# Kernel tuning notes

Hardware: AMD Instinct MI355X
Metric: run time of the kernel (lower is better)

The kernel has to match this reference:

```python
import jax, jax.numpy as jnp
import numpy as np
import math

EMBED_DIM = 1024
NUM_HEADS = 16
QK_DIM = 64
SCALE = 1.0 / math.sqrt(QK_DIM)  # beta=None -> 1/sqrt(qk_dim)


def setup_inputs() -> dict:
    key = jax.random.key(0)
    k1, k2, k3 = jax.random.split(key, 3)
    hidden_states = jax.random.normal(k1, (2, 2048, EMBED_DIM), dtype=jnp.float32)
    # nn.init.normal_(std=0.002)
    query_proj = 0.002 * jax.random.normal(k2, (NUM_HEADS, QK_DIM, EMBED_DIM), dtype=jnp.float32)
    key_proj = 0.002 * jax.random.normal(k3, (NUM_HEADS, QK_DIM, EMBED_DIM), dtype=jnp.float32)
    query_bias = jnp.zeros((QK_DIM,), dtype=jnp.float32)
    key_bias = jnp.zeros((QK_DIM,), dtype=jnp.float32)
    return {
        "hidden_states": hidden_states,
        "query_proj": query_proj,
        "key_proj": key_proj,
        "query_bias": query_bias,
        "key_bias": key_bias,
    }


def reference(hidden_states, query_proj, key_proj, query_bias, key_bias):
    # queries/keys: [b, n, h, q]
    queries = jnp.einsum("bnd,hqd->bnhq", hidden_states, query_proj) + query_bias
    keys = jnp.einsum("bnd,hqd->bnhq", hidden_states, key_proj) + key_bias
    # scores: [b, h, n, m]
    scores = jnp.einsum("bnhq,bmhq->bhnm", queries, keys)
    # energy: -sum logsumexp over last dim, divided by scale
    lse = jax.scipy.special.logsumexp(SCALE * scores, axis=-1)
    return -jnp.sum(lse) / SCALE
```

## Files before the change

kernel.cpp:

```cpp
#include <hip/hip_runtime.h>
#include <hip/hip_bf16.h>
#include <stdint.h>


typedef __bf16 bf16_t;
typedef bf16_t bf16x8 __attribute__((ext_vector_type(8)));
typedef float f32x4 __attribute__((ext_vector_type(4)));
typedef float f32x16 __attribute__((ext_vector_type(16)));

#define MFMA16(a,b,c) __builtin_amdgcn_mfma_f32_16x16x32_bf16(a,b,c,0,0,0)
#define MFMA32(a,b,c) __builtin_amdgcn_mfma_f32_32x32x16_bf16(a,b,c,0,0,0)
#define GLL16(g, l) __builtin_amdgcn_global_load_lds(                       \
    (const __attribute__((address_space(1))) void*)(g),                     \
    (__attribute__((address_space(3))) void*)(l), 16, 0, 0)

static constexpr int SEQ = 2048, BATCH = 2, EMBED = 1024, NH = 16, QKD = 64;
static constexpr int M_TOT = BATCH * SEQ;
static constexpr int N_TOT = 2 * NH * QKD;
static constexpr float C1 = 0.125f * 1.44269504088896340736f;

__global__ __launch_bounds__(256) void cvt_kernel(
    const float* __restrict__ hs, const float* __restrict__ qp,
    const float* __restrict__ kp, bf16_t* __restrict__ hsb,
    bf16_t* __restrict__ projb)
{
    int i = blockIdx.x * 256 + threadIdx.x;
    const float* src; bf16_t* dst;
    if (i < 524288) { src = hs + (size_t)i * 8; dst = hsb + (size_t)i * 8; }
    else {
        int j = i - 524288;
        dst = projb + (size_t)j * 8;
        src = (j < 131072) ? qp + (size_t)j * 8 : kp + (size_t)(j - 131072) * 8;
    }
    f32x4 a = ((const f32x4*)src)[0], b = ((const f32x4*)src)[1];
    bf16x8 r;
    r[0]=(bf16_t)a[0]; r[1]=(bf16_t)a[1]; r[2]=(bf16_t)a[2]; r[3]=(bf16_t)a[3];
    r[4]=(bf16_t)b[0]; r[5]=(bf16_t)b[1]; r[6]=(bf16_t)b[2]; r[7]=(bf16_t)b[3];
    *(bf16x8*)dst = r;
}

__global__ __launch_bounds__(256) void proj_kernel(
    const bf16_t* __restrict__ A, const bf16_t* __restrict__ B,
    const float* __restrict__ qb, const float* __restrict__ kb,
    bf16_t* __restrict__ C)
{
    __shared__ __align__(16) char sA[2][16384];
    __shared__ __align__(16) char sB[2][16384];
    const int t = threadIdx.x, lane = t & 63, wv = t >> 6;
    const int bid = blockIdx.x;
    const int xcd = bid & 7, idx = bid >> 3;
    const int am0 = (xcd * 4 + (idx >> 4)) * 128;
    const int bn0 = (idx & 15) * 128;
    const int wr = wv >> 1, wc = wv & 1;
    const int l15 = lane & 15, g = lane >> 4;

    const int srow = wv * 8 + (lane >> 3);
    const int sgr  = (lane & 7) ^ ((lane >> 3) & 7);
    const bf16_t* ga = A + (size_t)(am0 + srow) * EMBED + sgr * 8;
    const bf16_t* gb = B + (size_t)(bn0 + srow) * EMBED + sgr * 8;
    const int lbase = wv * 1024;

    f32x4 acc[4][4] = {};

#pragma unroll
    for (int is = 0; is < 4; ++is) {
        GLL16(ga + (size_t)is * 32 * EMBED, &sA[0][lbase + is * 4096]);
        GLL16(gb + (size_t)is * 32 * EMBED, &sB[0][lbase + is * 4096]);
    }
    __syncthreads();

    int cur = 0;
    for (int kk = 0; kk < EMBED; kk += 64) {
        if (kk + 64 < EMBED) {
#pragma unroll
            for (int is = 0; is < 4; ++is) {
                GLL16(ga + kk + 64 + (size_t)is * 32 * EMBED, &sA[cur ^ 1][lbase + is * 4096]);
                GLL16(gb + kk + 64 + (size_t)is * 32 * EMBED, &sB[cur ^ 1][lbase + is * 4096]);
            }
        }
#pragma unroll
        for (int s = 0; s < 2; ++s) {
            bf16x8 af[4], bfv[4];
#pragma unroll
            for (int mt = 0; mt < 4; ++mt) {
                int row = wr * 64 + mt * 16 + l15;
                af[mt] = *(const bf16x8*)&sA[cur][row * 128 + 16 * (((s << 2) | g) ^ (row & 7))];
            }
#pragma unroll
            for (int nt = 0; nt < 4; ++nt) {
                int row = wc * 64 + nt * 16 + l15;
                bfv[nt] = *(const bf16x8*)&sB[cur][row * 128 + 16 * (((s << 2) | g) ^ (row & 7))];
            }
#pragma unroll
            for (int mt = 0; mt < 4; ++mt)
#pragma unroll
                for (int nt = 0; nt < 4; ++nt)
                    acc[mt][nt] = MFMA16(af[mt], bfv[nt], acc[mt][nt]);
        }
        __syncthreads();
        cur ^= 1;
    }

#pragma unroll
    for (int nt = 0; nt < 4; ++nt) {
        int col = bn0 + wc * 64 + nt * 16 + l15;
        float bias, scale;
        if (col < NH * QKD) { bias = qb[col & 63]; scale = C1; }
        else                { bias = kb[col & 63]; scale = 1.0f; }
#pragma unroll
        for (int mt = 0; mt < 4; ++mt)
#pragma unroll
            for (int j = 0; j < 4; ++j) {
                int row = am0 + wr * 64 + mt * 16 + g * 4 + j;
                C[(size_t)row * N_TOT + col] = (bf16_t)((acc[mt][nt][j] + bias) * scale);
            }
    }
}

__global__ __launch_bounds__(256) void lse_kernel(
    const bf16_t* __restrict__ qk, float* __restrict__ partials)
{
    __shared__ float rows_s[4][128];
    __shared__ float ws[4];
    const int t = threadIdx.x, lane = t & 63, wv = t >> 6;
    const int bid = blockIdx.x;
    const int xcd = bid & 7, idx = bid >> 3;
    const int pair = xcd * 4 + (idx >> 4);
    const int tile = idx & 15;
    const int b = pair >> 4, h = pair & 15;
    const int qr0 = tile * 128;
    const int l31 = lane & 31, g5 = lane >> 5;
    const size_t base = (size_t)b * SEQ;

    bf16x8 qf[4][4];
#pragma unroll
    for (int mt = 0; mt < 4; ++mt) {
        const bf16_t* qp_ = qk + (base + qr0 + mt * 32 + l31) * N_TOT + h * QKD + g5 * 8;
#pragma unroll
        for (int kf = 0; kf < 4; ++kf)
            qf[mt][kf] = *(const bf16x8*)(qp_ + kf * 16);
    }

    const bf16_t* kb_ = qk + (base + wv * 512 + l31) * N_TOT + NH * QKD + h * QKD + g5 * 8;

    float sume[4] = {0.f, 0.f, 0.f, 0.f};

    bf16x8 kv[4];
#pragma unroll
    for (int kf = 0; kf < 4; ++kf) kv[kf] = *(const bf16x8*)(kb_ + kf * 16);

    for (int ct = 0; ct < 16; ++ct) {
        bf16x8 kn[4];
        const bf16_t* kn_p = kb_ + (size_t)((ct < 15 ? ct + 1 : 15) * 32) * N_TOT;
#pragma unroll
        for (int kf = 0; kf < 4; ++kf) kn[kf] = *(const bf16x8*)(kn_p + kf * 16);

        f32x16 sacc[4];
#pragma unroll
        for (int mt = 0; mt < 4; ++mt) {
            f32x16 z = {};
            sacc[mt] = z;
#pragma unroll
            for (int kf = 0; kf < 4; ++kf)
                sacc[mt] = MFMA32(kv[kf], qf[mt][kf], sacc[mt]);
        }
#pragma unroll
        for (int mt = 0; mt < 4; ++mt) {
            float e = 0.f;
#pragma unroll
            for (int j = 0; j < 16; ++j)
                e += __builtin_amdgcn_exp2f(sacc[mt][j]);
            sume[mt] += e;
        }
#pragma unroll
        for (int kf = 0; kf < 4; ++kf) kv[kf] = kn[kf];
    }

#pragma unroll
    for (int mt = 0; mt < 4; ++mt) {
        float v = sume[mt] + __shfl_xor(sume[mt], 32);
        if (g5 == 0) rows_s[wv][mt * 32 + l31] = v;
    }
    __syncthreads();

    float lg = 0.f;
    if (t < 128) {
        float tot = rows_s[0][t] + rows_s[1][t] + rows_s[2][t] + rows_s[3][t];
        lg = __builtin_amdgcn_logf(tot);
    }
#pragma unroll
    for (int m = 1; m < 64; m <<= 1) lg += __shfl_xor(lg, m);
    if (lane == 0) ws[wv] = lg;
    __syncthreads();
    if (t == 0)
        partials[bid] = ws[0] + ws[1] + ws[2] + ws[3];
}

__global__ __launch_bounds__(256) void final_kernel(
    const float* __restrict__ partials, int n, float* __restrict__ out)
{
    float s = 0.f;
    for (int i = threadIdx.x; i < n; i += 256) s += partials[i];
#pragma unroll
    for (int m = 1; m < 64; m <<= 1) s += __shfl_xor(s, m);
    __shared__ float wsf[4];
    const int wave = threadIdx.x >> 6, lane = threadIdx.x & 63;
    if (lane == 0) wsf[wave] = s;
    __syncthreads();
    if (threadIdx.x == 0)
        out[0] = -8.0f * 0.69314718055994530942f * (wsf[0] + wsf[1] + wsf[2] + wsf[3]);
}

extern "C" void kernel_launch(void* const* d_in, const int* in_sizes, int n_in,
                              void* d_out, int out_size, void* d_ws, size_t ws_size,
                              hipStream_t stream)
{
    const float* hs = (const float*)d_in[0];
    const float* qp = (const float*)d_in[1];
    const float* kp = (const float*)d_in[2];
    const float* qb = (const float*)d_in[3];
    const float* kb = (const float*)d_in[4];

    bf16_t* hsb   = (bf16_t*)d_ws;
    bf16_t* projb = hsb + (size_t)M_TOT * EMBED;
    bf16_t* qkb   = projb + (size_t)N_TOT * EMBED;
    float*  partials = (float*)(qkb + (size_t)M_TOT * N_TOT);
    float*  out = (float*)d_out;

    cvt_kernel<<<3072, 256, 0, stream>>>(hs, qp, kp, hsb, projb);
    proj_kernel<<<512, 256, 0, stream>>>(hsb, projb, qb, kb, qkb);
    lse_kernel<<<512, 256, 0, stream>>>(qkb, partials);
    final_kernel<<<1, 256, 0, stream>>>(partials, 512, out);
}
```

Measured before the change: 58.71 us.

## Interleave GEMM staging loads with MFMA quarters and raise MFMA priority

Restructures the projection GEMM main loop into four quadrant steps per K tile. Each step issues part of the next tile's global-to-LDS loads and reads a subset of fragments, with explicit vmcnt waits, s_barriers and sched barriers so the memory traffic overlaps the MFMAs. The wave-to-tile mapping changes to interleaved 16-row/column strips, and launch bounds request two blocks per CU. It also wraps MFMA sections in s_setprio in both the GEMM and the LSE kernel. This adds fragile hand-scheduled synchronisation whose correctness depends on exact vmcnt counts and barrier placement.

Measured after the change: 60.25 us. 1.03x slower.

```diff
diff --git a/kernel.cpp b/kernel.cpp
--- a/kernel.cpp
+++ b/kernel.cpp
@@ -13,6 +13,11 @@
 #define GLL16(g, l) __builtin_amdgcn_global_load_lds(                       \
     (const __attribute__((address_space(1))) void*)(g),                     \
     (__attribute__((address_space(3))) void*)(l), 16, 0, 0)
+
+#define SB0     __builtin_amdgcn_sched_barrier(0)
+#define BARRIER __builtin_amdgcn_s_barrier()
+#define VMCNT4  do { SB0; asm volatile("s_waitcnt vmcnt(4)" ::: "memory"); SB0; } while(0)
+#define LGKM0   do { asm volatile("s_waitcnt lgkmcnt(0)" ::: "memory"); SB0; } while(0)
 
 static constexpr int SEQ = 2048, BATCH = 2, EMBED = 1024, NH = 16, QKD = 64;
 static constexpr int M_TOT = BATCH * SEQ;
@@ -39,7 +44,7 @@
     *(bf16x8*)dst = r;
 }
 
-__global__ __launch_bounds__(256) void proj_kernel(
+__global__ __launch_bounds__(256, 2) void proj_kernel(
     const bf16_t* __restrict__ A, const bf16_t* __restrict__ B,
     const float* __restrict__ qb, const float* __restrict__ kb,
     bf16_t* __restrict__ C)
@@ -54,56 +59,76 @@
     const int wr = wv >> 1, wc = wv & 1;
     const int l15 = lane & 15, g = lane >> 4;
 
-    const int srow = wv * 8 + (lane >> 3);
-    const int sgr  = (lane & 7) ^ ((lane >> 3) & 7);
-    const bf16_t* ga = A + (size_t)(am0 + srow) * EMBED + sgr * 8;
-    const bf16_t* gb = B + (size_t)(bn0 + srow) * EMBED + sgr * 8;
-    const int lbase = wv * 1024;
-
+    const int sgr = (lane & 7) ^ ((lane >> 3) & 7);
+    const bf16_t* gA[2][2];
+    const bf16_t* gB[2][2];
+#pragma unroll
+    for (int h = 0; h < 2; ++h)
+#pragma unroll
+        for (int l = 0; l < 2; ++l) {
+            int row = h * 64 + l * 32 + wv * 8 + (lane >> 3);
+            gA[h][l] = A + (size_t)(am0 + row) * EMBED + 8 * sgr;
+            gB[h][l] = B + (size_t)(bn0 + row) * EMBED + 8 * sgr;
+        }
+
+#define STAGE_A(BUF,H,KK) do {                                              \
+    GLL16(gA[H][0] + (KK), &sA[BUF][(H)*8192 +        wv*1024]);            \
+    GLL16(gA[H][1] + (KK), &sA[BUF][(H)*8192 + 4096 + wv*1024]); } while(0)
+#define STAGE_B(BUF,H,KK) do {                                              \
+    GLL16(gB[H][0] + (KK), &sB[BUF][(H)*8192 +        wv*1024]);            \
+    GLL16(gB[H][1] + (KK), &sB[BUF][(H)*8192 + 4096 + wv*1024]); } while(0)
+#define READ_A(BUF,MT,S,DST) do { int row_ = (MT)*32 + wr*16 + l15;         \
+    DST = *(const bf16x8*)&sA[BUF][row_*128 + 16*((((S)<<2)|g) ^ (row_&7))]; } while(0)
+#define READ_B(BUF,NT,S,DST) do { int row_ = (NT)*32 + wc*16 + l15;         \
+    DST = *(const bf16x8*)&sB[BUF][row_*128 + 16*((((S)<<2)|g) ^ (row_&7))]; } while(0)
+#define MFMA_Q(MT0,NT0) do {                                                \
+    __builtin_amdgcn_s_setprio(1);                                          \
+    _Pragma("unroll") for (int s_ = 0; s_ < 2; ++s_)                        \
+    _Pragma("unroll") for (int m_ = 0; m_ < 2; ++m_)                        \
+    _Pragma("unroll") for (int n_ = 0; n_ < 2; ++n_)                        \
+        acc[(MT0)+m_][(NT0)+n_] =                                           \
+            MFMA16(aF[(MT0)+m_][s_], bF[(NT0)+n_][s_], acc[(MT0)+m_][(NT0)+n_]); \
+    __builtin_amdgcn_s_setprio(0); SB0; } while(0)
+
+    bf16x8 aF[4][2], bF[4][2];
     f32x4 acc[4][4] = {};
 
-#pragma unroll
-    for (int is = 0; is < 4; ++is) {
-        GLL16(ga + (size_t)is * 32 * EMBED, &sA[0][lbase + is * 4096]);
-        GLL16(gb + (size_t)is * 32 * EMBED, &sB[0][lbase + is * 4096]);
-    }
-    __syncthreads();
-
-    int cur = 0;
-    for (int kk = 0; kk < EMBED; kk += 64) {
-        if (kk + 64 < EMBED) {
-#pragma unroll
-            for (int is = 0; is < 4; ++is) {
-                GLL16(ga + kk + 64 + (size_t)is * 32 * EMBED, &sA[cur ^ 1][lbase + is * 4096]);
-                GLL16(gb + kk + 64 + (size_t)is * 32 * EMBED, &sB[cur ^ 1][lbase + is * 4096]);
-            }
-        }
-#pragma unroll
-        for (int s = 0; s < 2; ++s) {
-            bf16x8 af[4], bfv[4];
-#pragma unroll
-            for (int mt = 0; mt < 4; ++mt) {
-                int row = wr * 64 + mt * 16 + l15;
-                af[mt] = *(const bf16x8*)&sA[cur][row * 128 + 16 * (((s << 2) | g) ^ (row & 7))];
-            }
-#pragma unroll
-            for (int nt = 0; nt < 4; ++nt) {
-                int row = wc * 64 + nt * 16 + l15;
-                bfv[nt] = *(const bf16x8*)&sB[cur][row * 128 + 16 * (((s << 2) | g) ^ (row & 7))];
-            }
-#pragma unroll
-            for (int mt = 0; mt < 4; ++mt)
-#pragma unroll
-                for (int nt = 0; nt < 4; ++nt)
-                    acc[mt][nt] = MFMA16(af[mt], bfv[nt], acc[mt][nt]);
-        }
-        __syncthreads();
-        cur ^= 1;
+    STAGE_A(0, 0, 0); STAGE_B(0, 0, 0); STAGE_A(0, 1, 0); STAGE_B(0, 1, 0);
+
+#define TILE(BUF, TT) do {                                                  \
+    const int nk_ = ((TT) < 15 ? (TT) + 1 : 15) * 64;                       \
+            \
+    VMCNT4; BARRIER; SB0;                                                   \
+    STAGE_A(BUF^1, 0, nk_);                                                 \
+    READ_A(BUF,0,0,aF[0][0]); READ_A(BUF,0,1,aF[0][1]);                     \
+    READ_A(BUF,1,0,aF[1][0]); READ_A(BUF,1,1,aF[1][1]);                     \
+    READ_B(BUF,0,0,bF[0][0]); READ_B(BUF,0,1,bF[0][1]);                     \
+    READ_B(BUF,1,0,bF[1][0]); READ_B(BUF,1,1,bF[1][1]);                     \
+    LGKM0; MFMA_Q(0, 0);                                                    \
+                                                        \
+    VMCNT4; BARRIER; SB0;                                                   \
+    STAGE_B(BUF^1, 0, nk_);                                                 \
+    READ_A(BUF,2,0,aF[2][0]); READ_A(BUF,2,1,aF[2][1]);                     \
+    READ_A(BUF,3,0,aF[3][0]); READ_A(BUF,3,1,aF[3][1]);                     \
+    LGKM0; MFMA_Q(2, 0);                                                    \
+                                \
+    VMCNT4; BARRIER; SB0;                                                   \
+    STAGE_A(BUF^1, 1, nk_);                                                 \
+    READ_B(BUF,2,0,bF[2][0]); READ_B(BUF,2,1,bF[2][1]);                     \
+    READ_B(BUF,3,0,bF[3][0]); READ_B(BUF,3,1,bF[3][1]);                     \
+    LGKM0; MFMA_Q(2, 2);                                                    \
+                         \
+    STAGE_B(BUF^1, 1, nk_);                                                 \
+    MFMA_Q(0, 2); } while(0)
+
+    for (int tp = 0; tp < 8; ++tp) {
+        TILE(0, tp * 2);
+        TILE(1, tp * 2 + 1);
     }
 
 #pragma unroll
     for (int nt = 0; nt < 4; ++nt) {
-        int col = bn0 + wc * 64 + nt * 16 + l15;
+        int col = bn0 + nt * 32 + wc * 16 + l15;
         float bias, scale;
         if (col < NH * QKD) { bias = qb[col & 63]; scale = C1; }
         else                { bias = kb[col & 63]; scale = 1.0f; }
@@ -111,10 +136,16 @@
         for (int mt = 0; mt < 4; ++mt)
 #pragma unroll
             for (int j = 0; j < 4; ++j) {
-                int row = am0 + wr * 64 + mt * 16 + g * 4 + j;
+                int row = am0 + mt * 32 + wr * 16 + g * 4 + j;
                 C[(size_t)row * N_TOT + col] = (bf16_t)((acc[mt][nt][j] + bias) * scale);
             }
     }
+#undef TILE
+#undef MFMA_Q
+#undef READ_A
+#undef READ_B
+#undef STAGE_A
+#undef STAGE_B
 }
 
 __global__ __launch_bounds__(256) void lse_kernel(
@@ -156,6 +187,7 @@
         for (int kf = 0; kf < 4; ++kf) kn[kf] = *(const bf16x8*)(kn_p + kf * 16);
 
         f32x16 sacc[4];
+        __builtin_amdgcn_s_setprio(1);
 #pragma unroll
         for (int mt = 0; mt < 4; ++mt) {
             f32x16 z = {};
@@ -164,6 +196,7 @@
             for (int kf = 0; kf < 4; ++kf)
                 sacc[mt] = MFMA32(kv[kf], qf[mt][kf], sacc[mt]);
         }
+        __builtin_amdgcn_s_setprio(0);
 #pragma unroll
         for (int mt = 0; mt < 4; ++mt) {
             float e = 0.f;
```

## Stage K tiles through LDS with async loads and fuse final reduction

Applied to the files above, without the earlier changes.

The LSE kernel now stages the K tiles into double-buffered, XOR-swizzled shared memory using global_load_lds. Before, each wave read K directly from global memory in strided 16-byte loads and prefetched only through registers. MFMA issue priority is raised with s_setprio. The separate final reduction kernel is replaced by a last-block-done pattern built on an atomic counter, which removes one launch but adds a memset and a fence.

After: 82.92 us. 1.41x slower.

```diff
diff --git a/kernel.cpp b/kernel.cpp
--- a/kernel.cpp
+++ b/kernel.cpp
@@ -18,6 +18,7 @@
 static constexpr int M_TOT = BATCH * SEQ;
 static constexpr int N_TOT = 2 * NH * QKD;
 static constexpr float C1 = 0.125f * 1.44269504088896340736f;
+static constexpr int NBLK = 512;
 
 __global__ __launch_bounds__(256) void cvt_kernel(
     const float* __restrict__ hs, const float* __restrict__ qp,
@@ -56,8 +57,8 @@
 
     const int srow = wv * 8 + (lane >> 3);
     const int sgr  = (lane & 7) ^ ((lane >> 3) & 7);
-    const bf16_t* ga = A + (size_t)(am0 + srow) * EMBED + sgr * 8;
-    const bf16_t* gb = B + (size_t)(bn0 + srow) * EMBED + sgr * 8;
+    const bf16_t* ga = A + (size_t)(am0 + srow) * EMBED + 8 * sgr;
+    const bf16_t* gb = B + (size_t)(bn0 + srow) * EMBED + 8 * sgr;
     const int lbase = wv * 1024;
 
     f32x4 acc[4][4] = {};
@@ -118,10 +119,13 @@
 }
 
 __global__ __launch_bounds__(256) void lse_kernel(
-    const bf16_t* __restrict__ qk, float* __restrict__ partials)
-{
+    const bf16_t* __restrict__ qk, float* __restrict__ red,
+    unsigned* __restrict__ cnt, float* __restrict__ out)
+{
+    __shared__ __align__(16) char sK[2][32768];
     __shared__ float rows_s[4][128];
-    __shared__ float ws[4];
+    __shared__ float wsf[4];
+    __shared__ int lastflag;
     const int t = threadIdx.x, lane = t & 63, wv = t >> 6;
     const int bid = blockIdx.x;
     const int xcd = bid & 7, idx = bid >> 3;
@@ -131,6 +135,7 @@
     const int qr0 = tile * 128;
     const int l31 = lane & 31, g5 = lane >> 5;
     const size_t base = (size_t)b * SEQ;
+    const int KOFF = NH * QKD + h * QKD;
 
     bf16x8 qf[4][4];
 #pragma unroll
@@ -141,41 +146,55 @@
             qf[mt][kf] = *(const bf16x8*)(qp_ + kf * 16);
     }
 
-    const bf16_t* kb_ = qk + (base + wv * 512 + l31) * N_TOT + NH * QKD + h * QKD + g5 * 8;
+    const int sgr = (lane & 7) ^ ((lane >> 3) & 7);
+    const bf16_t* kbase = qk + (base + wv * 8 + (lane >> 3)) * N_TOT + KOFF + sgr * 8;
+    const int lbase = wv * 1024;
+
+#define STAGE_K(BUF, KC) do {                                               \
+    _Pragma("unroll") for (int l_ = 0; l_ < 8; ++l_)                        \
+        GLL16(kbase + (size_t)((KC) + l_ * 32) * N_TOT,                     \
+              &sK[BUF][l_ * 4096 + lbase]); } while(0)
 
     float sume[4] = {0.f, 0.f, 0.f, 0.f};
 
-    bf16x8 kv[4];
-#pragma unroll
-    for (int kf = 0; kf < 4; ++kf) kv[kf] = *(const bf16x8*)(kb_ + kf * 16);
-
-    for (int ct = 0; ct < 16; ++ct) {
-        bf16x8 kn[4];
-        const bf16_t* kn_p = kb_ + (size_t)((ct < 15 ? ct + 1 : 15) * 32) * N_TOT;
-#pragma unroll
-        for (int kf = 0; kf < 4; ++kf) kn[kf] = *(const bf16x8*)(kn_p + kf * 16);
-
-        f32x16 sacc[4];
-#pragma unroll
-        for (int mt = 0; mt < 4; ++mt) {
-            f32x16 z = {};
-            sacc[mt] = z;
+    STAGE_K(0, 0);
+    for (int c = 0; c < 8; ++c) {
+        const int buf = c & 1;
+        __syncthreads();
+        if (c < 7) STAGE_K(buf ^ 1, (c + 1) * 256);
+
+#pragma unroll
+        for (int i = 0; i < 2; ++i) {
+            const int rl = (wv * 2 + i) * 32 + l31;
+            bf16x8 kv[4];
 #pragma unroll
             for (int kf = 0; kf < 4; ++kf)
-                sacc[mt] = MFMA32(kv[kf], qf[mt][kf], sacc[mt]);
+                kv[kf] = *(const bf16x8*)&sK[buf][rl * 128 + 16 * ((kf * 2 + g5) ^ (rl & 7))];
+
+            f32x16 sacc[4];
+            __builtin_amdgcn_s_setprio(1);
+#pragma unroll
+            for (int mt = 0; mt < 4; ++mt) {
+                f32x16 z = {};
+                sacc[mt] = z;
+#pragma unroll
+                for (int kf = 0; kf < 4; ++kf)
+                    sacc[mt] = MFMA32(kv[kf], qf[mt][kf], sacc[mt]);
+            }
+            __builtin_amdgcn_s_setprio(0);
+#pragma unroll
+            for (int mt = 0; mt < 4; ++mt) {
+                float e = 0.f;
+#pragma unroll
+                for (int j = 0; j < 16; ++j)
+                    e += __builtin_amdgcn_exp2f(sacc[mt][j]);
+                sume[mt] += e;
+            }
         }
-#pragma unroll
-        for (int mt = 0; mt < 4; ++mt) {
-            float e = 0.f;
-#pragma unroll
-            for (int j = 0; j < 16; ++j)
-                e += __builtin_amdgcn_exp2f(sacc[mt][j]);
-            sume[mt] += e;
-        }
-#pragma unroll
-        for (int kf = 0; kf < 4; ++kf) kv[kf] = kn[kf];
-    }
-
+    }
+#undef STAGE_K
+
+    __syncthreads();
 #pragma unroll
     for (int mt = 0; mt < 4; ++mt) {
         float v = sume[mt] + __shfl_xor(sume[mt], 32);
@@ -190,25 +209,27 @@
     }
 #pragma unroll
     for (int m = 1; m < 64; m <<= 1) lg += __shfl_xor(lg, m);
-    if (lane == 0) ws[wv] = lg;
-    __syncthreads();
-    if (t == 0)
-        partials[bid] = ws[0] + ws[1] + ws[2] + ws[3];
-}
-
-__global__ __launch_bounds__(256) void final_kernel(
-    const float* __restrict__ partials, int n, float* __restrict__ out)
-{
-    float s = 0.f;
-    for (int i = threadIdx.x; i < n; i += 256) s += partials[i];
-#pragma unroll
-    for (int m = 1; m < 64; m <<= 1) s += __shfl_xor(s, m);
-    __shared__ float wsf[4];
-    const int wave = threadIdx.x >> 6, lane = threadIdx.x & 63;
-    if (lane == 0) wsf[wave] = s;
-    __syncthreads();
-    if (threadIdx.x == 0)
-        out[0] = -8.0f * 0.69314718055994530942f * (wsf[0] + wsf[1] + wsf[2] + wsf[3]);
+    if (lane == 0) wsf[wv] = lg;
+    __syncthreads();
+
+    if (t == 0) {
+        red[bid] = wsf[0] + wsf[1] + wsf[2] + wsf[3];
+        __threadfence();
+        unsigned d = atomicAdd(cnt, 1u);
+        lastflag = (d == NBLK - 1);
+    }
+    __syncthreads();
+
+    if (lastflag) {
+        __threadfence();
+        float s = red[t] + red[t + 256];
+#pragma unroll
+        for (int m = 1; m < 64; m <<= 1) s += __shfl_xor(s, m);
+        if (lane == 0) wsf[wv] = s;
+        __syncthreads();
+        if (t == 0)
+            out[0] = -8.0f * 0.69314718055994530942f * (wsf[0] + wsf[1] + wsf[2] + wsf[3]);
+    }
 }
 
 extern "C" void kernel_launch(void* const* d_in, const int* in_sizes, int n_in,
@@ -224,11 +245,12 @@
     bf16_t* hsb   = (bf16_t*)d_ws;
     bf16_t* projb = hsb + (size_t)M_TOT * EMBED;
     bf16_t* qkb   = projb + (size_t)N_TOT * EMBED;
-    float*  partials = (float*)(qkb + (size_t)M_TOT * N_TOT);
-    float*  out = (float*)d_out;
-
+    float*  red   = (float*)(qkb + (size_t)M_TOT * N_TOT);
+    unsigned* cnt = (unsigned*)(red + NBLK);
+    float*  out   = (float*)d_out;
+
+    hipMemsetAsync(cnt, 0, sizeof(unsigned), stream);
     cvt_kernel<<<3072, 256, 0, stream>>>(hs, qp, kp, hsb, projb);
-    proj_kernel<<<512, 256, 0, stream>>>(hsb, projb, qb, kb, qkb);
-    lse_kernel<<<512, 256, 0, stream>>>(qkb, partials);
-    final_kernel<<<1, 256, 0, stream>>>(partials, 512, out);
-}
+    proj_kernel<<<NBLK, 256, 0, stream>>>(hsb, projb, qb, kb, qkb);
+    lse_kernel<<<NBLK, 256, 0, stream>>>(qkb, red, cnt, out);
+}
```
